# Optimization experiments

Measured on AMD Instinct MI355X. Metric: run time of the kernel, lower is better.

Reference implementation:

```python
import jax, jax.numpy as jnp
import numpy as np

N_INST = 50
TAU = 1.0
ALPHA = 1.0


def smooth_top1_svm(logits, targets, n_classes=2):
    # SmoothTop1SVM (topk.svm): tau * logsumexp((s + alpha*(1-onehot_y))/tau) - s_y, mean over batch
    delta = ALPHA * (1.0 - jax.nn.one_hot(targets, n_classes, dtype=logits.dtype))
    lse = TAU * jax.nn.logsumexp((logits + delta) / TAU, axis=1)
    s_y = jnp.take_along_axis(logits, targets[:, None], axis=1)[:, 0]
    return jnp.mean(lse - s_y)


def setup_inputs() -> dict:
    key = jax.random.key(0)
    ks = jax.random.split(key, 14)
    N, E, L, D, C = 131072, 1024, 512, 256, 2
    g = lambda k, shp: jax.random.normal(k, shp, dtype=jnp.float32) * (shp[-1] ** -0.5)
    return {
        "x": jax.random.normal(ks[0], (N, E), dtype=jnp.float32),
        "label": 0,  # static python int: class with in-class instance eval
        "Wc": g(ks[1], (L, E)), "bc": jnp.zeros((L,), jnp.float32),
        "Wv": g(ks[2], (D, L)), "bv": jnp.zeros((D,), jnp.float32),
        "Wu": g(ks[3], (D, L)), "bu": jnp.zeros((D,), jnp.float32),
        "Wa": g(ks[4], (C, D)), "ba": jnp.zeros((C,), jnp.float32),
        "Winst": g(ks[5], (C, 2, L)), "binst": jnp.zeros((C, 2), jnp.float32),
        "Wbag": g(ks[6], (C, L)), "bbag": jnp.zeros((C,), jnp.float32),
    }


def reference(x, label, Wc, bc, Wv, bv, Wu, bu, Wa, ba, Winst, binst, Wbag, bbag):
    C = Wa.shape[0]
    # gated attention backbone
    h = jax.nn.relu(x @ Wc.T + bc)                      # [N, L] compressed features
    a = jnp.tanh(h @ Wv.T + bv)                          # [N, D]
    b = jax.nn.sigmoid(h @ Wu.T + bu)                    # [N, D]
    A = (a * b) @ Wa.T + ba                              # [N, C]
    x_att = A.T                                          # [C, N]
    raw_attention = x_att
    attn = jax.nn.softmax(x_att, axis=1)                 # [C, N]

    # instance-level eval (in-class branch only; subtyping=False skips others)
    total_loss = jnp.zeros((), jnp.float32)
    for c in range(C):
        if c == label:
            attn_c = attn[c]                             # [N]
            _, top_p = jax.lax.top_k(attn_c, N_INST)     # most attended
            _, top_n = jax.lax.top_k(-attn_c, N_INST)    # least attended
            inst = jnp.concatenate([h[top_p], h[top_n]], axis=0)   # [2*n_inst, L]
            logits_i = inst @ Winst[c].T + binst[c]                 # [2*n_inst, 2]
            targets = jnp.concatenate([jnp.ones((N_INST,), jnp.int32),
                                       jnp.zeros((N_INST,), jnp.int32)])
            total_loss = total_loss + smooth_top1_svm(logits_i, targets)

    # bag-level: multi-branch, one Linear(L,1) per class
    bag_rep = attn @ h                                   # [C, L]
    logits = (jnp.sum(bag_rep * Wbag, axis=1) + bbag)[None, :]  # [1, C]
    y_proba = jax.nn.softmax(logits, axis=1)
    return (logits, y_proba, raw_attention, total_loss)
```

## Files before the change

### kernel.cpp

```cpp
#include <hip/hip_runtime.h>
#include <hip/hip_bf16.h>
#include <math.h>

#define NROWS 131072
#define E 1024
#define L 512
#define DD 256
#define NI 50
#define CAP 2048
#define NBINS 16384

typedef __attribute__((ext_vector_type(8))) short bf16x8;
typedef __attribute__((ext_vector_type(4))) float f32x4;

__device__ __forceinline__ unsigned short f2bf(float f) {
  unsigned u = __float_as_uint(f);
  unsigned r = (u + 0x7FFFu + ((u >> 16) & 1u)) >> 16;
  return (unsigned short)r;
}
__device__ __forceinline__ float bf2f(unsigned short b) {
  return __uint_as_float(((unsigned)b) << 16);
}
__device__ __forceinline__ float frcp(float x) { return __builtin_amdgcn_rcpf(x); }
__device__ __forceinline__ float fsig(float x) { return frcp(1.0f + __expf(-x)); }
__device__ __forceinline__ float ftanh(float x) { return 2.0f * frcp(1.0f + __expf(-2.0f * x)) - 1.0f; }
__device__ __forceinline__ unsigned encf(float f) {
  unsigned u = __float_as_uint(f);
  return (u & 0x80000000u) ? ~u : (u | 0x80000000u);
}
__device__ __forceinline__ float decf(unsigned e) {
  unsigned b = (e & 0x80000000u) ? (e & 0x7FFFFFFFu) : ~e;
  return __uint_as_float(b);
}

#define GLDS16(gp, lp)                                                        \
  __builtin_amdgcn_global_load_lds(                                           \
      (const __attribute__((address_space(1))) void*)(gp),                    \
      (__attribute__((address_space(3))) void*)(lp), 16, 0, 0)

__global__ void k0_init(const float* __restrict__ Wc, const float* __restrict__ Wv,
                        const float* __restrict__ Wu,
                        unsigned short* __restrict__ WcB, unsigned short* __restrict__ W2B,
                        float* __restrict__ Aws, float* __restrict__ tws,
                        unsigned* __restrict__ hist,
                        float* __restrict__ scalF, unsigned* __restrict__ scalU) {
  const int i0 = blockIdx.x * blockDim.x + threadIdx.x;
  const int str = gridDim.x * blockDim.x;
  if (i0 < 4) scalF[i0] = 0.f;
  if (i0 < 16) scalU[i0] = (i0 == 0) ? 0xFFFFFFFFu : 0u;
  for (int k = i0; k < NBINS; k += str) hist[k] = 0u;
  for (int k = i0; k < NROWS * 2; k += str) { Aws[k] = 0.f; tws[k] = 0.f; }
  for (int k = i0; k < L * E; k += str) WcB[k] = f2bf(Wc[k]);
  for (int k = i0; k < DD * L; k += str) { W2B[k] = f2bf(Wv[k]); W2B[DD * L + k] = f2bf(Wu[k]); }
}

__global__ __launch_bounds__(256) void k1_gemm1(const float* __restrict__ x,
                                                const unsigned short* __restrict__ WcB,
                                                const float* __restrict__ bc,
                                                const float* __restrict__ Wbag,
                                                unsigned short* __restrict__ hB,
                                                float* __restrict__ tws) {
  __shared__ __align__(16) unsigned short xs[128 * 64];
  __shared__ __align__(16) unsigned short wt[256 * 64];
  const int tid = threadIdx.x;
  const int lane = tid & 63;
  const int wv = tid >> 6;
  const int cbk = blockIdx.x & 1;
  const int rbk = blockIdx.x >> 1;
  const int row0 = rbk << 7;
  const int col0 = cbk << 8;
  const int wr = wv >> 1, wc = wv & 1;
  const int q = lane >> 4, c15 = lane & 15;

  f32x4 acc[4][8];
#pragma unroll
  for (int i = 0; i < 4; ++i)
#pragma unroll
    for (int j = 0; j < 8; ++j) acc[i][j] = {0.f, 0.f, 0.f, 0.f};

  for (int kk = 0; kk < E; kk += 64) {
    __syncthreads();
#pragma unroll
    for (int i = 0; i < 8; ++i) {
      const int g = (wv << 3) + i;
      const int slot = (g << 6) + lane;
      const int j = slot >> 3;
      const int s = slot & 7;
      const int k8 = s ^ (j & 7);
      GLDS16(WcB + (size_t)(col0 + j) * E + kk + (k8 << 3), wt + (g << 9));
    }
#pragma unroll
    for (int i = 0; i < 4; ++i) {
      const int ci = (i << 8) + tid;
      const int r = ci >> 3;
      const int s = ci & 7;
      const float* gp = x + (size_t)(row0 + r) * E + kk + (s << 3);
      const float4 v0 = *(const float4*)gp;
      const float4 v1 = *(const float4*)(gp + 4);
      bf16x8 hv;
      hv[0] = (short)f2bf(v0.x); hv[1] = (short)f2bf(v0.y);
      hv[2] = (short)f2bf(v0.z); hv[3] = (short)f2bf(v0.w);
      hv[4] = (short)f2bf(v1.x); hv[5] = (short)f2bf(v1.y);
      hv[6] = (short)f2bf(v1.z); hv[7] = (short)f2bf(v1.w);
      *(bf16x8*)(xs + (r << 6) + ((s ^ (r & 7)) << 3)) = hv;
    }
    __syncthreads();
#pragma unroll
    for (int ks = 0; ks < 2; ++ks) {
      const int ch = (ks << 2) + q;
      bf16x8 af[4];
#pragma unroll
      for (int mt = 0; mt < 4; ++mt) {
        const int rr = (wr << 6) + (mt << 4) + c15;
        af[mt] = *(const bf16x8*)(xs + (rr << 6) + ((ch ^ (rr & 7)) << 3));
      }
#pragma unroll
      for (int nt = 0; nt < 8; ++nt) {
        const int jj = (wc << 7) + (nt << 4) + c15;
        const bf16x8 bb = *(const bf16x8*)(wt + (jj << 6) + ((ch ^ (jj & 7)) << 3));
#pragma unroll
        for (int mt = 0; mt < 4; ++mt)
          acc[mt][nt] = __builtin_amdgcn_mfma_f32_16x16x32_bf16(af[mt], bb, acc[mt][nt], 0, 0, 0);
      }
    }
  }
  float bias[8], wb0[8], wb1[8];
#pragma unroll
  for (int nt = 0; nt < 8; ++nt) {
    const int colg = col0 + (wc << 7) + (nt << 4) + c15;
    bias[nt] = bc[colg];
    wb0[nt] = Wbag[colg];
    wb1[nt] = Wbag[L + colg];
  }
#pragma unroll
  for (int mt = 0; mt < 4; ++mt) {
#pragma unroll
    for (int r = 0; r < 4; ++r) {
      const int rowg = row0 + (wr << 6) + (mt << 4) + (q << 2) + r;
      float tp0 = 0.f, tp1 = 0.f;
#pragma unroll
      for (int nt = 0; nt < 8; ++nt) {
        const int colg = col0 + (wc << 7) + (nt << 4) + c15;
        float v = acc[mt][nt][r] + bias[nt];
        v = v > 0.f ? v : 0.f;
        tp0 += v * wb0[nt];
        tp1 += v * wb1[nt];
        const unsigned short hb = f2bf(v);
        const unsigned short ob = (unsigned short)__shfl_xor((int)hb, 1, 64);
        if (!(lane & 1)) {
          *(unsigned*)(hB + (size_t)rowg * L + colg) = (unsigned)hb | ((unsigned)ob << 16);
        }
      }
#pragma unroll
      for (int off = 1; off < 16; off <<= 1) {
        tp0 += __shfl_xor(tp0, off, 64);
        tp1 += __shfl_xor(tp1, off, 64);
      }
      if (c15 == 0) {
        atomicAdd(&tws[(rowg << 1)], tp0);
        atomicAdd(&tws[(rowg << 1) + 1], tp1);
      }
    }
  }
}

__global__ __launch_bounds__(256) void k2_gemm2(const unsigned short* __restrict__ hB,
                                                const unsigned short* __restrict__ W2B,
                                                const float* __restrict__ bv,
                                                const float* __restrict__ bu,
                                                const float* __restrict__ Wa,
                                                float* __restrict__ Aws) {
  __shared__ __align__(16) unsigned short hs[128 * 64];
  __shared__ __align__(16) unsigned short wt[256 * 64];
  const int tid = threadIdx.x, lane = tid & 63, wv = tid >> 6;
  const int cbk = blockIdx.x & 1, rbk = blockIdx.x >> 1;
  const int row0 = rbk << 7;
  const int q = lane >> 4, c15 = lane & 15;

  f32x4 acc[2][16];
#pragma unroll
  for (int i = 0; i < 2; ++i)
#pragma unroll
    for (int j = 0; j < 16; ++j) acc[i][j] = {0.f, 0.f, 0.f, 0.f};

  for (int kk = 0; kk < L; kk += 64) {
    __syncthreads();
#pragma unroll
    for (int i = 0; i < 4; ++i) {
      const int g = (wv << 2) + i;
      const int slot = (g << 6) + lane;
      const int j = slot >> 3;
      const int s = slot & 7;
      const int k8 = s ^ (j & 7);
      GLDS16(hB + (size_t)(row0 + j) * L + kk + (k8 << 3), hs + (g << 9));
    }
#pragma unroll
    for (int i = 0; i < 8; ++i) {
      const int g = (wv << 3) + i;
      const int slot = (g << 6) + lane;
      const int j = slot >> 3;
      const int s = slot & 7;
      const int k8 = s ^ (j & 7);
      const int w2row = (j < 128) ? ((cbk << 7) + j) : (DD + (cbk << 7) + (j - 128));
      GLDS16(W2B + (size_t)w2row * L + kk + (k8 << 3), wt + (g << 9));
    }
    __syncthreads();
#pragma unroll
    for (int ks = 0; ks < 2; ++ks) {
      const int ch = (ks << 2) + q;
      bf16x8 af[2];
#pragma unroll
      for (int mt = 0; mt < 2; ++mt) {
        const int rr = (wv << 5) + (mt << 4) + c15;
        af[mt] = *(const bf16x8*)(hs + (rr << 6) + ((ch ^ (rr & 7)) << 3));
      }
#pragma unroll
      for (int nt = 0; nt < 16; ++nt) {
        const int jj = (nt << 4) + c15;
        const bf16x8 bb = *(const bf16x8*)(wt + (jj << 6) + ((ch ^ (jj & 7)) << 3));
        acc[0][nt] = __builtin_amdgcn_mfma_f32_16x16x32_bf16(af[0], bb, acc[0][nt], 0, 0, 0);
        acc[1][nt] = __builtin_amdgcn_mfma_f32_16x16x32_bf16(af[1], bb, acc[1][nt], 0, 0, 0);
      }
    }
  }
  float wa0[8], wa1[8], bvv[8], buv[8];
#pragma unroll
  for (int nt = 0; nt < 8; ++nt) {
    const int d = (cbk << 7) + (nt << 4) + c15;
    wa0[nt] = Wa[d]; wa1[nt] = Wa[DD + d];
    bvv[nt] = bv[d]; buv[nt] = bu[d];
  }
#pragma unroll
  for (int mt = 0; mt < 2; ++mt) {
#pragma unroll
    for (int r = 0; r < 4; ++r) {
      const int rowg = row0 + (wv << 5) + (mt << 4) + (q << 2) + r;
      float p0 = 0.f, p1 = 0.f;
#pragma unroll
      for (int nt = 0; nt < 8; ++nt) {
        const float av = ftanh(acc[mt][nt][r] + bvv[nt]);
        const float bx = fsig(acc[mt][nt + 8][r] + buv[nt]);
        const float ab = av * bx;
        p0 += ab * wa0[nt];
        p1 += ab * wa1[nt];
      }
#pragma unroll
      for (int off = 1; off < 16; off <<= 1) {
        p0 += __shfl_xor(p0, off, 64);
        p1 += __shfl_xor(p1, off, 64);
      }
      if (c15 == 0) {
        atomicAdd(&Aws[(rowg << 1)], p0);
        atomicAdd(&Aws[(rowg << 1) + 1], p1);
      }
    }
  }
}

__global__ void k3a_elem(const float* __restrict__ Aws, const float* __restrict__ tws,
                         const float* __restrict__ ba, const int* __restrict__ lblp,
                         float* __restrict__ out,
                         float* __restrict__ scalF, unsigned* __restrict__ scalU) {
  const int row = blockIdx.x * 256 + threadIdx.x;
  const int lane = threadIdx.x & 63;
  const float2 Ap = ((const float2*)Aws)[row];
  const float2 tp = ((const float2*)tws)[row];
  const float A0 = Ap.x + ba[0];
  const float A1 = Ap.y + ba[1];
  out[4 + row] = A0;
  out[4 + NROWS + row] = A1;
  const float e0 = __expf(A0), e1 = __expf(A1);
  float z0 = e0, z1 = e1, s0 = e0 * tp.x, s1 = e1 * tp.y;
  const int lbl = *lblp;
  unsigned u = encf(lbl ? A1 : A0);
  unsigned umin = u, umax = u;
#pragma unroll
  for (int off = 1; off < 64; off <<= 1) {
    z0 += __shfl_xor(z0, off, 64);
    z1 += __shfl_xor(z1, off, 64);
    s0 += __shfl_xor(s0, off, 64);
    s1 += __shfl_xor(s1, off, 64);
    const unsigned om = (unsigned)__shfl_xor((int)umin, off, 64);
    const unsigned oM = (unsigned)__shfl_xor((int)umax, off, 64);
    umin = umin < om ? umin : om;
    umax = umax > oM ? umax : oM;
  }
  if (lane == 0) {
    atomicAdd(&scalF[0], z0); atomicAdd(&scalF[1], z1);
    atomicAdd(&scalF[2], s0); atomicAdd(&scalF[3], s1);
    atomicMin(&scalU[0], umin);
    atomicMax(&scalU[1], umax);
  }
}

__global__ __launch_bounds__(1024) void k3b_hist(const float* __restrict__ out,
                                                 const int* __restrict__ lblp,
                                                 const unsigned* __restrict__ scalU,
                                                 unsigned* __restrict__ hist) {
  __shared__ unsigned lh[NBINS];
  const int tid = threadIdx.x;
  for (int i = tid; i < NBINS; i += 1024) lh[i] = 0u;
  __syncthreads();
  const int lbl = *lblp;
  const int row = blockIdx.x * 1024 + tid;
  const float A = out[4 + (size_t)lbl * NROWS + row];
  const float mn = decf(scalU[0]);
  const float mx = decf(scalU[1]);
  const float scale = (mx > mn) ? (float)(NBINS - 1) / (mx - mn) : 0.f;
  int bin = (int)((A - mn) * scale);
  bin = bin < 0 ? 0 : (bin > NBINS - 1 ? NBINS - 1 : bin);
  atomicAdd(&lh[bin], 1u);
  __syncthreads();
  for (int i = tid; i < NBINS; i += 1024) {
    const unsigned c = lh[i];
    if (c) atomicAdd(&hist[i], c);
  }
}

__global__ void k4_scan(const unsigned* __restrict__ hist,
                        const float* __restrict__ scalF,
                        unsigned* __restrict__ scalU,
                        const float* __restrict__ bbag,
                        float* __restrict__ out) {
  __shared__ unsigned csum[256];
  const int t = threadIdx.x;
  unsigned s = 0;
  for (int b = 0; b < 64; ++b) s += hist[t * 64 + b];
  csum[t] = s;
  __syncthreads();
  if (t == 0) {
    unsigned acc = 0; int ch = 255;
    for (; ch > 0; --ch) { if (acc + csum[ch] >= NI) break; acc += csum[ch]; }
    unsigned binHi = 0;
    for (int b = ch * 64 + 63; b >= ch * 64; --b) { acc += hist[b]; if (acc >= NI) { binHi = (unsigned)b; break; } }
    scalU[6] = binHi;
    acc = 0; int cl = 0;
    for (; cl < 255; ++cl) { if (acc + csum[cl] >= NI) break; acc += csum[cl]; }
    unsigned binLo = NBINS - 1;
    for (int b = cl * 64; b < cl * 64 + 64; ++b) { acc += hist[b]; if (acc >= NI) { binLo = (unsigned)b; break; } }
    scalU[7] = binLo;
    const float l0 = scalF[2] / scalF[0] + bbag[0];
    const float l1 = scalF[3] / scalF[1] + bbag[1];
    const float m = fmaxf(l0, l1);
    const float e0 = __expf(l0 - m), e1 = __expf(l1 - m);
    const float inv = 1.0f / (e0 + e1);
    out[0] = l0; out[1] = l1; out[2] = e0 * inv; out[3] = e1 * inv;
  }
}

__global__ void k5_collect(const float* __restrict__ out,
                           const int* __restrict__ lblp,
                           unsigned* __restrict__ scalU,
                           unsigned* __restrict__ chK, unsigned* __restrict__ chI,
                           unsigned* __restrict__ clK, unsigned* __restrict__ clI) {
  const int binHi = (int)scalU[6], binLo = (int)scalU[7];
  const float mn = decf(scalU[0]);
  const float mx = decf(scalU[1]);
  const float scale = (mx > mn) ? (float)(NBINS - 1) / (mx - mn) : 0.f;
  const int lbl = *lblp;
  const float* Ap = out + 4 + (size_t)lbl * NROWS;
  const int n = blockIdx.x * 256 + threadIdx.x;
  const float A = Ap[n];
  int bin = (int)((A - mn) * scale);
  bin = bin < 0 ? 0 : (bin > NBINS - 1 ? NBINS - 1 : bin);
  const unsigned u = encf(A);
  if (bin >= binHi) { unsigned p = atomicAdd(&scalU[4], 1u); if (p < CAP) { chK[p] = u; chI[p] = (unsigned)n; } }
  if (bin <= binLo) { unsigned p = atomicAdd(&scalU[5], 1u); if (p < CAP) { clK[p] = u; clI[p] = (unsigned)n; } }
}

__global__ __launch_bounds__(256) void k6_loss(const unsigned* __restrict__ scalU,
                                               const unsigned* __restrict__ chK, const unsigned* __restrict__ chI,
                                               const unsigned* __restrict__ clK, const unsigned* __restrict__ clI,
                                               const unsigned short* __restrict__ hB,
                                               const float* __restrict__ Winst,
                                               const float* __restrict__ binst,
                                               const int* __restrict__ lblp,
                                               float* __restrict__ out) {
  __shared__ unsigned kH[CAP], iH[CAP], kL[CAP], iL[CAP];
  __shared__ int selT[NI], selB[NI];
  __shared__ float lossA[256];
  const int t = threadIdx.x;
  const int lbl = *lblp;
  const unsigned cH = scalU[4], cL = scalU[5];
  const int nH = (int)(cH < CAP ? cH : CAP);
  const int nL = (int)(cL < CAP ? cL : CAP);
  if (t < NI) { selT[t] = 0; selB[t] = 0; }
  for (int i = t; i < nH; i += 256) { kH[i] = chK[i]; iH[i] = chI[i]; }
  for (int i = t; i < nL; i += 256) { kL[i] = clK[i]; iL[i] = clI[i]; }
  __syncthreads();
  for (int c = t; c < nH; c += 256) {
    const unsigned k = kH[c], id = iH[c];
    int rank = 0;
    for (int j = 0; j < nH; ++j) rank += (kH[j] > k) || (kH[j] == k && iH[j] < id);
    if (rank < NI) selT[rank] = (int)id;
  }
  for (int c = t; c < nL; c += 256) {
    const unsigned k = kL[c], id = iL[c];
    int rank = 0;
    for (int j = 0; j < nL; ++j) rank += (kL[j] < k) || (kL[j] == k && iL[j] < id);
    if (rank < NI) selB[rank] = (int)id;
  }
  __syncthreads();
  float loss = 0.f;
  if (t < 2 * NI) {
    const int idx = (t < NI) ? selT[t] : selB[t - NI];
    const int target = (t < NI) ? 1 : 0;
    const unsigned short* hp = hB + (size_t)idx * L;
    const float* w0 = Winst + (size_t)lbl * 2 * L;
    const float* w1 = w0 + L;
    float l0 = binst[lbl * 2 + 0], l1 = binst[lbl * 2 + 1];
    for (int k = 0; k < L; ++k) {
      const float hv = bf2f(hp[k]);
      l0 += hv * w0[k];
      l1 += hv * w1[k];
    }
    const float z0 = l0 + (target ? 1.0f : 0.0f);
    const float z1 = l1 + (target ? 0.0f : 1.0f);
    const float m = fmaxf(z0, z1);
    const float lse = m + logf(__expf(z0 - m) + __expf(z1 - m));
    loss = lse - (target ? l1 : l0);
  }
  lossA[t] = loss;
  __syncthreads();
  for (int sft = 128; sft; sft >>= 1) {
    if (t < sft) lossA[t] += lossA[t + sft];
    __syncthreads();
  }
  if (t == 0) out[4 + 2 * NROWS] = lossA[0] / 100.0f;
}

extern "C" void kernel_launch(void* const* d_in, const int* in_sizes, int n_in,
                              void* d_out, int out_size, void* d_ws, size_t ws_size,
                              hipStream_t stream) {
  const float* x     = (const float*)d_in[0];
  const int*   lbl   = (const int*)d_in[1];
  const float* Wc    = (const float*)d_in[2];
  const float* bc    = (const float*)d_in[3];
  const float* Wv    = (const float*)d_in[4];
  const float* bv    = (const float*)d_in[5];
  const float* Wu    = (const float*)d_in[6];
  const float* bu    = (const float*)d_in[7];
  const float* Wa    = (const float*)d_in[8];
  const float* ba    = (const float*)d_in[9];
  const float* Winst = (const float*)d_in[10];
  const float* binst = (const float*)d_in[11];
  const float* Wbag  = (const float*)d_in[12];
  const float* bbag  = (const float*)d_in[13];
  float* out = (float*)d_out;
  char* ws = (char*)d_ws;

  unsigned short* hB   = (unsigned short*)(ws);
  unsigned short* WcB  = (unsigned short*)(ws + 134217728LL);
  unsigned short* W2B  = (unsigned short*)(ws + 135266304LL);
  float*          Aws  = (float*)(ws + 135790592LL);
  float*          tws  = (float*)(ws + 136839168LL);
  unsigned*       hist = (unsigned*)(ws + 137887744LL);
  float*          scalF= (float*)(ws + 137953280LL);
  unsigned*       scalU= (unsigned*)(ws + 137953344LL);
  unsigned*       chK  = (unsigned*)(ws + 137953408LL);
  unsigned*       chI  = chK + CAP;
  unsigned*       clK  = chI + CAP;
  unsigned*       clI  = clK + CAP;

  k0_init<<<2048, 256, 0, stream>>>(Wc, Wv, Wu, WcB, W2B, Aws, tws, hist, scalF, scalU);
  k1_gemm1<<<2048, 256, 0, stream>>>(x, WcB, bc, Wbag, hB, tws);
  k2_gemm2<<<2048, 256, 0, stream>>>(hB, W2B, bv, bu, Wa, Aws);
  k3a_elem<<<512, 256, 0, stream>>>(Aws, tws, ba, lbl, out, scalF, scalU);
  k3b_hist<<<128, 1024, 0, stream>>>(out, lbl, scalU, hist);
  k4_scan<<<1, 256, 0, stream>>>(hist, scalF, scalU, bbag, out);
  k5_collect<<<512, 256, 0, stream>>>(out, lbl, scalU, chK, chI, clK, clI);
  k6_loss<<<1, 256, 0, stream>>>(scalU, chK, chI, clK, clI, hB, Winst, binst, lbl, out);
}
```

Baseline: 1.310 ms.

## Stream fp32 x tiles directly to LDS and convert to bf16 at fragment load

The first GEMM now loads the fp32 x tile straight into LDS with asynchronous global_load_lds, where it previously went through registers with a manual bf16 rounding and store. The conversion to bf16 moves to fragment-load time using the packed v_cvt_pk_bf16_f32 instruction. The K step is halved to 32 so the fp32 tile fits in the same LDS budget, and both tiles get new XOR swizzles. This removes register staging and scalar rounding arithmetic, but it doubles the number of K-loop iterations and barriers, and the conversion is repeated by each wave column that reads the same rows.

Result: slower. 1.367 ms (+4.4%).

```diff
diff --git a/kernel.cpp b/kernel.cpp
--- a/kernel.cpp
+++ b/kernel.cpp
@@ -31,6 +31,11 @@
 __device__ __forceinline__ float decf(unsigned e) {
   unsigned b = (e & 0x80000000u) ? (e & 0x7FFFFFFFu) : ~e;
   return __uint_as_float(b);
+}
+__device__ __forceinline__ unsigned cvtpk(float a, float b) {
+  unsigned r;
+  asm("v_cvt_pk_bf16_f32 %0, %1, %2" : "=v"(r) : "v"(a), "v"(b));
+  return r;
 }
 
 #define GLDS16(gp, lp)                                                        \
@@ -60,8 +65,8 @@
                                                 const float* __restrict__ Wbag,
                                                 unsigned short* __restrict__ hB,
                                                 float* __restrict__ tws) {
-  __shared__ __align__(16) unsigned short xs[128 * 64];
-  __shared__ __align__(16) unsigned short wt[256 * 64];
+  __shared__ __align__(16) float xs[128 * 32];
+  __shared__ __align__(16) unsigned short wt[256 * 32];
   const int tid = threadIdx.x;
   const int lane = tid & 63;
   const int wv = tid >> 6;
@@ -78,50 +83,46 @@
 #pragma unroll
     for (int j = 0; j < 8; ++j) acc[i][j] = {0.f, 0.f, 0.f, 0.f};
 
-  for (int kk = 0; kk < E; kk += 64) {
+  for (int kk = 0; kk < E; kk += 32) {
     __syncthreads();
 #pragma unroll
-    for (int i = 0; i < 8; ++i) {
-      const int g = (wv << 3) + i;
+    for (int i = 0; i < 4; ++i) {
+      const int g = (wv << 2) + i;
       const int slot = (g << 6) + lane;
       const int j = slot >> 3;
       const int s = slot & 7;
-      const int k8 = s ^ (j & 7);
-      GLDS16(WcB + (size_t)(col0 + j) * E + kk + (k8 << 3), wt + (g << 9));
+      const int s4 = (s ^ (j & 7)) << 2;
+      GLDS16(x + (size_t)(row0 + j) * E + kk + s4, xs + (g << 8));
     }
 #pragma unroll
     for (int i = 0; i < 4; ++i) {
-      const int ci = (i << 8) + tid;
-      const int r = ci >> 3;
-      const int s = ci & 7;
-      const float* gp = x + (size_t)(row0 + r) * E + kk + (s << 3);
-      const float4 v0 = *(const float4*)gp;
-      const float4 v1 = *(const float4*)(gp + 4);
-      bf16x8 hv;
-      hv[0] = (short)f2bf(v0.x); hv[1] = (short)f2bf(v0.y);
-      hv[2] = (short)f2bf(v0.z); hv[3] = (short)f2bf(v0.w);
-      hv[4] = (short)f2bf(v1.x); hv[5] = (short)f2bf(v1.y);
-      hv[6] = (short)f2bf(v1.z); hv[7] = (short)f2bf(v1.w);
-      *(bf16x8*)(xs + (r << 6) + ((s ^ (r & 7)) << 3)) = hv;
+      const int g = (wv << 2) + i;
+      const int slot = (g << 6) + lane;
+      const int j = slot >> 2;
+      const int s = slot & 3;
+      const int s8 = (s ^ ((j >> 1) & 3)) << 3;
+      GLDS16(WcB + (size_t)(col0 + j) * E + kk + s8, wt + (g << 9));
     }
     __syncthreads();
-#pragma unroll
-    for (int ks = 0; ks < 2; ++ks) {
-      const int ch = (ks << 2) + q;
-      bf16x8 af[4];
-#pragma unroll
-      for (int mt = 0; mt < 4; ++mt) {
-        const int rr = (wr << 6) + (mt << 4) + c15;
-        af[mt] = *(const bf16x8*)(xs + (rr << 6) + ((ch ^ (rr & 7)) << 3));
-      }
-#pragma unroll
-      for (int nt = 0; nt < 8; ++nt) {
-        const int jj = (wc << 7) + (nt << 4) + c15;
-        const bf16x8 bb = *(const bf16x8*)(wt + (jj << 6) + ((ch ^ (jj & 7)) << 3));
-#pragma unroll
-        for (int mt = 0; mt < 4; ++mt)
-          acc[mt][nt] = __builtin_amdgcn_mfma_f32_16x16x32_bf16(af[mt], bb, acc[mt][nt], 0, 0, 0);
-      }
+    union { bf16x8 v; unsigned u[4]; } af[4];
+#pragma unroll
+    for (int mt = 0; mt < 4; ++mt) {
+      const int rr = (wr << 6) + (mt << 4) + c15;
+      const int r7 = rr & 7;
+      const f32x4 lo = *(const f32x4*)(xs + (rr << 5) + ((((q << 1)    ) ^ r7) << 2));
+      const f32x4 hi = *(const f32x4*)(xs + (rr << 5) + ((((q << 1) | 1) ^ r7) << 2));
+      af[mt].u[0] = cvtpk(lo[0], lo[1]);
+      af[mt].u[1] = cvtpk(lo[2], lo[3]);
+      af[mt].u[2] = cvtpk(hi[0], hi[1]);
+      af[mt].u[3] = cvtpk(hi[2], hi[3]);
+    }
+#pragma unroll
+    for (int nt = 0; nt < 8; ++nt) {
+      const int jj = (wc << 7) + (nt << 4) + c15;
+      const bf16x8 bb = *(const bf16x8*)(wt + (jj << 5) + ((q ^ ((jj >> 1) & 3)) << 3));
+#pragma unroll
+      for (int mt = 0; mt < 4; ++mt)
+        acc[mt][nt] = __builtin_amdgcn_mfma_f32_16x16x32_bf16(af[mt].v, bb, acc[mt][nt], 0, 0, 0);
     }
   }
   float bias[8], wb0[8], wb1[8];
```
